# Optimization experiments

Measured on AMD Instinct MI355X. Metric: run time of the kernel, lower is better.

## Reference

```python
import jax, jax.numpy as jnp
import numpy as np

HEADS = 4
HID = 32
IN = 128
OUT = 8
N = 50000
E = 1600000


def setup_inputs() -> dict:
    key = jax.random.key(0)
    ks = jax.random.split(key, 12)
    x = jax.random.normal(ks[0], (N, IN), dtype=jnp.float32)
    edge_index = jax.random.randint(ks[1], (2, E), 0, N, dtype=jnp.int64)
    s = 0.05
    W1 = jax.random.normal(ks[2], (IN, HEADS * HID), dtype=jnp.float32) * s
    att_src1 = jax.random.normal(ks[3], (HEADS, HID), dtype=jnp.float32) * s
    att_dst1 = jax.random.normal(ks[4], (HEADS, HID), dtype=jnp.float32) * s
    b1 = jnp.zeros((HEADS * HID,), dtype=jnp.float32)
    W2 = jax.random.normal(ks[5], (HEADS * HID, HEADS * HID), dtype=jnp.float32) * s
    att_src2 = jax.random.normal(ks[6], (HEADS, HID), dtype=jnp.float32) * s
    att_dst2 = jax.random.normal(ks[7], (HEADS, HID), dtype=jnp.float32) * s
    b2 = jnp.zeros((HEADS * HID,), dtype=jnp.float32)
    Wout = jax.random.normal(ks[8], (HEADS * HID, OUT), dtype=jnp.float32) * s
    bout = jnp.zeros((OUT,), dtype=jnp.float32)
    return {"x": x, "edge_index": edge_index, "W1": W1, "att_src1": att_src1,
            "att_dst1": att_dst1, "b1": b1, "W2": W2, "att_src2": att_src2,
            "att_dst2": att_dst2, "b2": b2, "Wout": Wout, "bout": bout}


def gat_conv(x, src, dst, W, att_src, att_dst, b):
    n = x.shape[0]
    h = (x @ W).reshape(n, HEADS, HID)              # [N,H,C]
    a_s = (h * att_src).sum(-1)                      # [N,H]
    a_d = (h * att_dst).sum(-1)                      # [N,H]
    e = jax.nn.leaky_relu(a_s[src] + a_d[dst], 0.2)  # [E,H]
    # scatter-softmax over incoming edges of each destination node
    m = jax.ops.segment_max(e, dst, num_segments=n)
    e = jnp.exp(e - m[dst])
    denom = jax.ops.segment_sum(e, dst, num_segments=n)
    alpha = e / (denom[dst] + 1e-16)                 # [E,H]
    msg = h[src] * alpha[:, :, None]                 # [E,H,C]
    out = jax.ops.segment_sum(msg, dst, num_segments=n)
    return out.reshape(n, HEADS * HID) + b


def reference(x, edge_index, W1, att_src1, att_dst1, b1, W2, att_src2, att_dst2, b2, Wout, bout):
    n = x.shape[0]
    # GATConv adds self-loops by default
    loops = jnp.arange(n, dtype=edge_index.dtype)
    src = jnp.concatenate([edge_index[0], loops])
    dst = jnp.concatenate([edge_index[1], loops])
    # dropout p=0.6 is identity in eval mode
    h = gat_conv(x, src, dst, W1, att_src1, att_dst1, b1)
    h = jax.nn.elu(h)
    h = gat_conv(h, src, dst, W2, att_src2, att_dst2, b2)
    return h @ Wout + bout
```

## Files before the change

kernel.cpp:

```cpp
#include <hip/hip_runtime.h>
#include <hip/hip_fp16.h>
#include <math.h>

#define N_NODES 50000
#define E_EDGES 1600000
#define NE_TOT  (E_EDGES + N_NODES)

#define BSH 7
#define NBKT ((N_NODES + 127) >> 7)
#define EPW 4096
#define NWA ((NE_TOT + EPW - 1) / EPW)

#define CH 128


__device__ __forceinline__ void gemm_att_body(
    int bid, int t, float* Wl, float* xs,
    const float* __restrict__ X, const float* __restrict__ W,
    const float* __restrict__ attS, const float* __restrict__ attD,
    __half* __restrict__ H16, float* __restrict__ a_s, float* __restrict__ a_d) {
    int g = t >> 5, cl = t & 31, c4 = cl * 4;
    int rowbase = bid * 32;
    float4 acc[4];
    #pragma unroll
    for (int rr = 0; rr < 4; rr++) acc[rr] = make_float4(0.f, 0.f, 0.f, 0.f);

    for (int kp = 0; kp < 2; kp++) {
        __syncthreads();
        #pragma unroll
        for (int j = 0; j < 8; j++) {
            int f4 = t + 256 * j;
            int kk = f4 >> 5, cg = f4 & 31;
            *(float4*)&Wl[kk * 128 + cg * 4] =
                *(const float4*)&W[(kp * 64 + kk) * 128 + cg * 4];
        }
        #pragma unroll
        for (int j = 0; j < 2; j++) {
            int f4 = t + 256 * j;
            int r = f4 >> 4, k4 = f4 & 15;
            int grow = rowbase + r;
            float4 xv = make_float4(0.f, 0.f, 0.f, 0.f);
            if (grow < N_NODES) xv = *(const float4*)&X[grow * 128 + kp * 64 + k4 * 4];
            *(float4*)&xs[r * 64 + k4 * 4] = xv;
        }
        __syncthreads();
        #pragma unroll
        for (int k4 = 0; k4 < 16; k4++) {
            float4 xv[4];
            #pragma unroll
            for (int rr = 0; rr < 4; rr++)
                xv[rr] = *(float4*)&xs[(g * 4 + rr) * 64 + k4 * 4];
            #pragma unroll
            for (int kk = 0; kk < 4; kk++) {
                float4 wv = *(float4*)&Wl[(k4 * 4 + kk) * 128 + c4];
                #pragma unroll
                for (int rr = 0; rr < 4; rr++) {
                    float xc = (kk == 0) ? xv[rr].x : (kk == 1) ? xv[rr].y
                             : (kk == 2) ? xv[rr].z : xv[rr].w;
                    acc[rr].x += xc * wv.x;
                    acc[rr].y += xc * wv.y;
                    acc[rr].z += xc * wv.z;
                    acc[rr].w += xc * wv.w;
                }
            }
        }
    }

    float4 as4 = *(const float4*)&attS[c4];
    float4 ad4 = *(const float4*)&attD[c4];
    int head = cl >> 3;
    #pragma unroll
    for (int rr = 0; rr < 4; rr++) {
        int grow = rowbase + g * 4 + rr;
        float4 a = acc[rr];
        if (grow < N_NODES) {
            __half2 lo = __floats2half2_rn(a.x, a.y);
            __half2 hi = __floats2half2_rn(a.z, a.w);
            uint2 pk;
            pk.x = *(unsigned int*)&lo;
            pk.y = *(unsigned int*)&hi;
            *(uint2*)&H16[(size_t)grow * 128 + c4] = pk;
        }
        float ps = a.x * as4.x + a.y * as4.y + a.z * as4.z + a.w * as4.w;
        float pd = a.x * ad4.x + a.y * ad4.y + a.z * ad4.z + a.w * ad4.w;
        ps += __shfl_xor(ps, 1); ps += __shfl_xor(ps, 2); ps += __shfl_xor(ps, 4);
        pd += __shfl_xor(pd, 1); pd += __shfl_xor(pd, 2); pd += __shfl_xor(pd, 4);
        if ((cl & 7) == 0 && grow < N_NODES) {
            a_s[grow * 4 + head] = ps;
            a_d[grow * 4 + head] = pd;
        }
    }
}

__global__ __launch_bounds__(256) void k_hist_gemm(
    const int* __restrict__ ei, int* __restrict__ histG,
    const float* __restrict__ X, const float* __restrict__ W,
    const float* __restrict__ attS, const float* __restrict__ attD,
    __half* __restrict__ H16, float* __restrict__ a_s, float* __restrict__ a_d) {
    __shared__ __align__(16) char smem[40960];
    int t = threadIdx.x;
    if (blockIdx.x < NWA) {
        int* h = (int*)smem;
        for (int i = t; i < NBKT; i += 256) h[i] = 0;
        __syncthreads();
        int base = blockIdx.x * EPW;
        #pragma unroll 4
        for (int j = 0; j < EPW / 256; j++) {
            int e = base + t + 256 * j;
            if (e < NE_TOT) {
                int d = (e < E_EDGES) ? ei[E_EDGES + e] : (e - E_EDGES);
                atomicAdd(&h[d >> BSH], 1);
            }
        }
        __syncthreads();
        for (int i = t; i < NBKT; i += 256) histG[blockIdx.x * NBKT + i] = h[i];
    } else {
        float* Wl = (float*)smem;
        float* xs = (float*)(smem + 32768);
        gemm_att_body(blockIdx.x - NWA, t, Wl, xs, X, W, attS, attD, H16, a_s, a_d);
    }
}

__global__ __launch_bounds__(256) void k_gemm_att(
    const float* __restrict__ X, const float* __restrict__ W,
    const float* __restrict__ attS, const float* __restrict__ attD,
    __half* __restrict__ H16, float* __restrict__ a_s, float* __restrict__ a_d) {
    __shared__ float Wl[64 * 128];
    __shared__ float xs[32 * 64];
    gemm_att_body(blockIdx.x, threadIdx.x, Wl, xs, X, W, attS, attD, H16, a_s, a_d);
}


__global__ __launch_bounds__(512) void k_bktscan(int* __restrict__ histG,
                                                 int* __restrict__ bktTotal) {
    __shared__ int sh[512];
    int b = blockIdx.x;
    int t = threadIdx.x;
    int v = (t < NWA) ? histG[t * NBKT + b] : 0;
    sh[t] = v;
    __syncthreads();
    for (int d = 1; d < 512; d <<= 1) {
        int x = (t >= d) ? sh[t - d] : 0;
        __syncthreads();
        sh[t] += x;
        __syncthreads();
    }
    if (t < NWA) histG[t * NBKT + b] = sh[t] - v;
    if (t == 511) bktTotal[b] = sh[511];
}

__global__ __launch_bounds__(512) void k_bktbase(const int* __restrict__ bktTotal,
                                                 int* __restrict__ bktBase,
                                                 int* __restrict__ row_start) {
    __shared__ int sc[512];
    int t = threadIdx.x;
    int v = (t < NBKT) ? bktTotal[t] : 0;
    sc[t] = v;
    __syncthreads();
    for (int d = 1; d < 512; d <<= 1) {
        int x = (t >= d) ? sc[t - d] : 0;
        __syncthreads();
        sc[t] += x;
        __syncthreads();
    }
    if (t < NBKT) bktBase[t] = sc[t] - v;
    if (t == NBKT - 1) { bktBase[NBKT] = sc[t]; row_start[N_NODES] = sc[t]; }
}

__global__ __launch_bounds__(256) void k_binscatter(const int* __restrict__ ei,
                                                    const int* __restrict__ histG,
                                                    const int* __restrict__ bktBase,
                                                    unsigned int* __restrict__ pairs) {
    __shared__ int lofs[NBKT];
    int t = threadIdx.x;
    for (int i = t; i < NBKT; i += 256)
        lofs[i] = bktBase[i] + histG[blockIdx.x * NBKT + i];
    __syncthreads();
    int base = blockIdx.x * EPW;
    #pragma unroll 4
    for (int j = 0; j < EPW / 256; j++) {
        int e = base + t + 256 * j;
        if (e < NE_TOT) {
            int s, d;
            if (e < E_EDGES) { s = ei[e]; d = ei[E_EDGES + e]; }
            else             { s = d = e - E_EDGES; }
            int pos = atomicAdd(&lofs[d >> BSH], 1);
            pairs[pos] = ((unsigned int)d << 16) | (unsigned int)s;
        }
    }
}

__global__ __launch_bounds__(256) void k_bucketsort(const unsigned int* __restrict__ pairs,
                                                    const int* __restrict__ bktBase,
                                                    int* __restrict__ row_start,
                                                    unsigned short* __restrict__ col) {
    __shared__ int cnt[1 << BSH];
    __shared__ int sc[1 << BSH];
    __shared__ int cur[1 << BSH];
    int b = blockIdx.x, t = threadIdx.x;
    int nbeg = b << BSH;
    int ebeg = bktBase[b], eend = bktBase[b + 1];
    if (t < (1 << BSH)) cnt[t] = 0;
    __syncthreads();
    for (int j = ebeg + t; j < eend; j += 256)
        atomicAdd(&cnt[(int)(pairs[j] >> 16) - nbeg], 1);
    __syncthreads();
    int v = (t < (1 << BSH)) ? cnt[t] : 0;
    if (t < (1 << BSH)) sc[t] = v;
    __syncthreads();
    for (int d = 1; d < (1 << BSH); d <<= 1) {
        int x = 0;
        if (t < (1 << BSH) && t >= d) x = sc[t - d];
        __syncthreads();
        if (t < (1 << BSH)) sc[t] += x;
        __syncthreads();
    }
    if (t < (1 << BSH)) {
        int pos = ebeg + sc[t] - v;
        cur[t] = pos;
        int node = nbeg + t;
        if (node < N_NODES) row_start[node] = pos;
    }
    __syncthreads();
    for (int j = ebeg + t; j < eend; j += 256) {
        unsigned int p = pairs[j];
        int pos = atomicAdd(&cur[(int)(p >> 16) - nbeg], 1);
        col[pos] = (unsigned short)(p & 0xFFFFu);
    }
}


__device__ inline float sel4(float4 v, int i) {
    float r = v.x;
    if (i == 1) r = v.y;
    if (i == 2) r = v.z;
    if (i == 3) r = v.w;
    return r;
}

__device__ inline float4 expleaky4(float4 a, float4 b) {
    float4 e, p;
    e.x = a.x + b.x; e.x = e.x > 0.f ? e.x : 0.2f * e.x; p.x = __expf(e.x);
    e.y = a.y + b.y; e.y = e.y > 0.f ? e.y : 0.2f * e.y; p.y = __expf(e.y);
    e.z = a.z + b.z; e.z = e.z > 0.f ? e.z : 0.2f * e.z; p.z = __expf(e.z);
    e.w = a.w + b.w; e.w = e.w > 0.f ? e.w : 0.2f * e.w; p.w = __expf(e.w);
    return p;
}

#define ACC8(q, raw)                                              \
    do {                                                          \
        const __half2* hp_ = (const __half2*)&(raw);              \
        float2 f0_ = __half22float2(hp_[0]);                      \
        float2 f1_ = __half22float2(hp_[1]);                      \
        float2 f2_ = __half22float2(hp_[2]);                      \
        float2 f3_ = __half22float2(hp_[3]);                      \
        acc8[0] = fmaf((q), f0_.x, acc8[0]);                      \
        acc8[1] = fmaf((q), f0_.y, acc8[1]);                      \
        acc8[2] = fmaf((q), f1_.x, acc8[2]);                      \
        acc8[3] = fmaf((q), f1_.y, acc8[3]);                      \
        acc8[4] = fmaf((q), f2_.x, acc8[4]);                      \
        acc8[5] = fmaf((q), f2_.y, acc8[5]);                      \
        acc8[6] = fmaf((q), f3_.x, acc8[6]);                      \
        acc8[7] = fmaf((q), f3_.y, acc8[7]);                      \
    } while (0)

template<int MODE>
__global__ __launch_bounds__(128) void k_agg(
    const __half* __restrict__ H16, const float* __restrict__ a_s,
    const float* __restrict__ a_d, const int* __restrict__ row_start,
    const unsigned short* __restrict__ col, const float* __restrict__ bias,
    float* __restrict__ Hout,
    const float* __restrict__ Wout, const float* __restrict__ bout,
    float* __restrict__ out) {
    __shared__ float4 eS[2][CH];
    __shared__ int    sS[2][CH];

    int wid = threadIdx.x >> 6;
    int lane = threadIdx.x & 63;
    int node = blockIdx.x * 2 + wid;
    if (node >= N_NODES) return;

    int eslot = lane >> 4, cl16 = lane & 15, head = cl16 >> 2;

    float wA[8], wB[8], bo0 = 0.f, bo1 = 0.f;
    if (MODE == 0) {
        int o0 = eslot * 2;
        #pragma unroll
        for (int k = 0; k < 8; k++) {
            wA[k] = Wout[(cl16 * 8 + k) * 8 + o0];
            wB[k] = Wout[(cl16 * 8 + k) * 8 + o0 + 1];
        }
        bo0 = bout[o0]; bo1 = bout[o0 + 1];
    }

    int beg = row_start[node], end = row_start[node + 1];
    int deg = end - beg;
    float4 ad4 = *(const float4*)&a_d[node * 4];
    float4* eA = eS[wid];
    int*    srcA = sS[wid];

    float4 s = make_float4(0.f, 0.f, 0.f, 0.f);
    for (int j = beg + lane; j < end; j += 64) {
        int src = (int)col[j];
        float4 av = *(const float4*)&a_s[src * 4];
        float4 p = expleaky4(av, ad4);
        int idx = j - beg;
        if (idx < CH) { srcA[idx] = src; eA[idx] = p; }
        s.x += p.x; s.y += p.y; s.z += p.z; s.w += p.w;
    }
    #pragma unroll
    for (int off = 32; off > 0; off >>= 1) {
        s.x += __shfl_xor(s.x, off);
        s.y += __shfl_xor(s.y, off);
        s.z += __shfl_xor(s.z, off);
        s.w += __shfl_xor(s.w, off);
    }
    float4 inv;
    inv.x = 1.f / (s.x + 1e-16f);
    inv.y = 1.f / (s.y + 1e-16f);
    inv.z = 1.f / (s.z + 1e-16f);
    inv.w = 1.f / (s.w + 1e-16f);

    const __half* hbase = H16 + cl16 * 8;
    const float* pA = (const float*)eA;
    float acc8[8];
    #pragma unroll
    for (int k = 0; k < 8; k++) acc8[k] = 0.f;

    int nst = min(deg, CH);
    int i = eslot;
    for (; i + 28 < nst; i += 32) {
        int sidx[8]; float qv[8]; float4 rv[8];
        #pragma unroll
        for (int k = 0; k < 8; k++) sidx[k] = srcA[i + 4 * k];
        #pragma unroll
        for (int k = 0; k < 8; k++) qv[k] = pA[(i + 4 * k) * 4 + head];
        #pragma unroll
        for (int k = 0; k < 8; k++)
            rv[k] = *(const float4*)(hbase + (size_t)sidx[k] * 128);
        #pragma unroll
        for (int k = 0; k < 8; k++) ACC8(qv[k], rv[k]);
    }
    for (; i + 12 < nst; i += 16) {
        int s0 = srcA[i];
        int s1 = srcA[i + 4];
        int s2 = srcA[i + 8];
        int s3 = srcA[i + 12];
        float q0 = pA[i * 4 + head];
        float q1 = pA[(i + 4) * 4 + head];
        float q2 = pA[(i + 8) * 4 + head];
        float q3 = pA[(i + 12) * 4 + head];
        float4 r0 = *(const float4*)(hbase + (size_t)s0 * 128);
        float4 r1 = *(const float4*)(hbase + (size_t)s1 * 128);
        float4 r2 = *(const float4*)(hbase + (size_t)s2 * 128);
        float4 r3 = *(const float4*)(hbase + (size_t)s3 * 128);
        ACC8(q0, r0);
        ACC8(q1, r1);
        ACC8(q2, r2);
        ACC8(q3, r3);
    }
    for (; i < nst; i += 4) {
        int src = srcA[i];
        float p = pA[i * 4 + head];
        float4 raw = *(const float4*)(hbase + (size_t)src * 128);
        ACC8(p, raw);
    }
    for (int cb = beg + CH; cb < end; cb += CH) {
        int cnt = min(end - cb, CH);
        for (int idx = lane; idx < cnt; idx += 64) {
            int src = (int)col[cb + idx];
            float4 av = *(const float4*)&a_s[src * 4];
            float4 p = expleaky4(av, ad4);
            srcA[idx] = src; eA[idx] = p;
        }
        for (int ii = eslot; ii < cnt; ii += 4) {
            int src = srcA[ii];
            float p = pA[ii * 4 + head];
            float4 raw = *(const float4*)(hbase + (size_t)src * 128);
            ACC8(p, raw);
        }
    }

    #pragma unroll
    for (int k = 0; k < 8; k++) {
        acc8[k] += __shfl_xor(acc8[k], 16);
        acc8[k] += __shfl_xor(acc8[k], 32);
    }

    float ih = sel4(inv, head);
    if (MODE == 1) {
        if (eslot == 0) {
            const float* bp = &bias[cl16 * 8];
            float o[8];
            #pragma unroll
            for (int k = 0; k < 8; k++) {
                o[k] = acc8[k] * ih + bp[k];
                o[k] = o[k] > 0.f ? o[k] : expm1f(o[k]);
            }
            float* op = &Hout[(size_t)node * 128 + cl16 * 8];
            *(float4*)&op[0] = make_float4(o[0], o[1], o[2], o[3]);
            *(float4*)&op[4] = make_float4(o[4], o[5], o[6], o[7]);
        }
    } else {
        const float* bp = &bias[cl16 * 8];
        float h2[8];
        #pragma unroll
        for (int k = 0; k < 8; k++) h2[k] = acc8[k] * ih + bp[k];
        float p0 = 0.f, p1 = 0.f;
        #pragma unroll
        for (int k = 0; k < 8; k++) {
            p0 = fmaf(h2[k], wA[k], p0);
            p1 = fmaf(h2[k], wB[k], p1);
        }
        #pragma unroll
        for (int d = 1; d <= 8; d <<= 1) {
            p0 += __shfl_xor(p0, d);
            p1 += __shfl_xor(p1, d);
        }
        if (cl16 == 0) {
            int o0 = eslot * 2;
            float2 ov = make_float2(p0 + bo0, p1 + bo1);
            *(float2*)&out[(size_t)node * 8 + o0] = ov;
        }
    }
}


extern "C" void kernel_launch(void* const* d_in, const int* in_sizes, int n_in,
                              void* d_out, int out_size, void* d_ws, size_t ws_size,
                              hipStream_t stream) {
    const float* x     = (const float*)d_in[0];
    const int*   ei    = (const int*)d_in[1];
    const float* W1    = (const float*)d_in[2];
    const float* attS1 = (const float*)d_in[3];
    const float* attD1 = (const float*)d_in[4];
    const float* b1    = (const float*)d_in[5];
    const float* W2    = (const float*)d_in[6];
    const float* attS2 = (const float*)d_in[7];
    const float* attD2 = (const float*)d_in[8];
    const float* b2    = (const float*)d_in[9];
    const float* Wout  = (const float*)d_in[10];
    const float* bout  = (const float*)d_in[11];
    float* out = (float*)d_out;

    char* ws = (char*)d_ws;
    size_t off = 0;
    auto alloc = [&](size_t bytes) -> void* {
        void* p = ws + off;
        off += (bytes + 255) & ~(size_t)255;
        return p;
    };
    float*          hB        = (float*)alloc((size_t)N_NODES * 128 * 4);
    __half*         h16       = (__half*)alloc((size_t)N_NODES * 128 * 2);
    float*          a_s       = (float*)alloc((size_t)N_NODES * 4 * 4);
    float*          a_d       = (float*)alloc((size_t)N_NODES * 4 * 4);
    int*            row_start = (int*)alloc((size_t)(N_NODES + 1) * 4);
    unsigned short* col       = (unsigned short*)alloc((size_t)NE_TOT * 2);
    int*            histG     = (int*)alloc((size_t)NWA * NBKT * 4);
    int*            bktTotal  = (int*)alloc((size_t)NBKT * 4);
    int*            bktBase   = (int*)alloc((size_t)(NBKT + 1) * 4);
    unsigned int*   pairs     = (unsigned int*)hB;

    int nbG = (N_NODES + 31) / 32;
    int nbA = (N_NODES + 1) / 2;

    k_hist_gemm<<<NWA + nbG, 256, 0, stream>>>(ei, histG, x, W1, attS1, attD1,
                                               h16, a_s, a_d);
    k_bktscan<<<NBKT, 512, 0, stream>>>(histG, bktTotal);
    k_bktbase<<<1, 512, 0, stream>>>(bktTotal, bktBase, row_start);
    k_binscatter<<<NWA, 256, 0, stream>>>(ei, histG, bktBase, pairs);
    k_bucketsort<<<NBKT, 256, 0, stream>>>(pairs, bktBase, row_start, col);

    k_agg<1><<<nbA, 128, 0, stream>>>(h16, a_s, a_d, row_start, col, b1, hB,
                                      Wout, bout, out);
    k_gemm_att<<<nbG, 256, 0, stream>>>(hB, W2, attS2, attD2, h16, a_s, a_d);
    k_agg<0><<<nbA, 128, 0, stream>>>(h16, a_s, a_d, row_start, col, b2, hB,
                                      Wout, bout, out);
}
```

Measured before the change: 286.9 us.

## Split each node's aggregation across two wavefronts with shared-memory reduction

The aggregation kernel now assigns two 64-lane wavefronts per destination node, in 256-thread blocks holding two nodes. The softmax denominator and feature accumulators are combined through shared memory. Overflow chunks for high-degree nodes are processed in lockstep with block-wide barriers. The output projection is computed only by the first wavefront's 16 lanes, reading Wout directly. This roughly doubles memory-level parallelism per node for the gather-bound loop, at the cost of added __syncthreads, a smaller unroll (4 loads per lane instead of 8), and idle lanes during the final projection.

```diff
diff --git a/kernel.cpp b/kernel.cpp
--- a/kernel.cpp
+++ b/kernel.cpp
@@ -265,7 +265,7 @@
     } while (0)
 
 template<int MODE>
-__global__ __launch_bounds__(128) void k_agg(
+__global__ __launch_bounds__(256) void k_agg(
     const __half* __restrict__ H16, const float* __restrict__ a_s,
     const float* __restrict__ a_d, const int* __restrict__ row_start,
     const unsigned short* __restrict__ col, const float* __restrict__ bias,
@@ -274,33 +274,24 @@
     float* __restrict__ out) {
     __shared__ float4 eS[2][CH];
     __shared__ int    sS[2][CH];
-
-    int wid = threadIdx.x >> 6;
+    __shared__ float  red[2][16][8];
+    __shared__ float4 sRed[2][2];
+    __shared__ int    chk[2];
+
+    int wv = threadIdx.x >> 6;
+    int nodeSlot = wv >> 1;
+    int wpair = wv & 1;
     int lane = threadIdx.x & 63;
-    int node = blockIdx.x * 2 + wid;
-    if (node >= N_NODES) return;
-
-    int eslot = lane >> 4, cl16 = lane & 15, head = cl16 >> 2;
-
-    float wA[8], wB[8], bo0 = 0.f, bo1 = 0.f;
-    if (MODE == 0) {
-        int o0 = eslot * 2;
-        #pragma unroll
-        for (int k = 0; k < 8; k++) {
-            wA[k] = Wout[(cl16 * 8 + k) * 8 + o0];
-            wB[k] = Wout[(cl16 * 8 + k) * 8 + o0 + 1];
-        }
-        bo0 = bout[o0]; bo1 = bout[o0 + 1];
-    }
+    int node = blockIdx.x * 2 + nodeSlot;
 
     int beg = row_start[node], end = row_start[node + 1];
     int deg = end - beg;
     float4 ad4 = *(const float4*)&a_d[node * 4];
-    float4* eA = eS[wid];
-    int*    srcA = sS[wid];
+    float4* eA = eS[nodeSlot];
+    int*    srcA = sS[nodeSlot];
 
     float4 s = make_float4(0.f, 0.f, 0.f, 0.f);
-    for (int j = beg + lane; j < end; j += 64) {
+    for (int j = beg + wpair * 64 + lane; j < end; j += 128) {
         int src = (int)col[j];
         float4 av = *(const float4*)&a_s[src * 4];
         float4 p = expleaky4(av, ad4);
@@ -315,12 +306,21 @@
         s.z += __shfl_xor(s.z, off);
         s.w += __shfl_xor(s.w, off);
     }
+    int myc = (deg > CH) ? (deg - CH + CH - 1) / CH : 0;
+    if (lane == 0) {
+        sRed[nodeSlot][wpair] = s;
+        if (wpair == 0) chk[nodeSlot] = myc;
+    }
+    __syncthreads();
+    float4 s0 = sRed[nodeSlot][0], s1 = sRed[nodeSlot][1];
     float4 inv;
-    inv.x = 1.f / (s.x + 1e-16f);
-    inv.y = 1.f / (s.y + 1e-16f);
-    inv.z = 1.f / (s.z + 1e-16f);
-    inv.w = 1.f / (s.w + 1e-16f);
-
+    inv.x = 1.f / (s0.x + s1.x + 1e-16f);
+    inv.y = 1.f / (s0.y + s1.y + 1e-16f);
+    inv.z = 1.f / (s0.z + s1.z + 1e-16f);
+    inv.w = 1.f / (s0.w + s1.w + 1e-16f);
+    int maxc = max(chk[0], chk[1]);
+
+    int slot8 = wpair * 4 + (lane >> 4), cl16 = lane & 15, head = cl16 >> 2;
     const __half* hbase = H16 + cl16 * 8;
     const float* pA = (const float*)eA;
     float acc8[8];
@@ -328,56 +328,52 @@
     for (int k = 0; k < 8; k++) acc8[k] = 0.f;
 
     int nst = min(deg, CH);
-    int i = eslot;
-    for (; i + 28 < nst; i += 32) {
-        int sidx[8]; float qv[8]; float4 rv[8];
-        #pragma unroll
-        for (int k = 0; k < 8; k++) sidx[k] = srcA[i + 4 * k];
-        #pragma unroll
-        for (int k = 0; k < 8; k++) qv[k] = pA[(i + 4 * k) * 4 + head];
-        #pragma unroll
-        for (int k = 0; k < 8; k++)
-            rv[k] = *(const float4*)(hbase + (size_t)sidx[k] * 128);
-        #pragma unroll
-        for (int k = 0; k < 8; k++) ACC8(qv[k], rv[k]);
-    }
-    for (; i + 12 < nst; i += 16) {
-        int s0 = srcA[i];
-        int s1 = srcA[i + 4];
-        int s2 = srcA[i + 8];
-        int s3 = srcA[i + 12];
+    int i = slot8;
+    for (; i + 24 < nst; i += 32) {
+        int t0 = srcA[i];
+        int t1 = srcA[i + 8];
+        int t2 = srcA[i + 16];
+        int t3 = srcA[i + 24];
         float q0 = pA[i * 4 + head];
-        float q1 = pA[(i + 4) * 4 + head];
-        float q2 = pA[(i + 8) * 4 + head];
-        float q3 = pA[(i + 12) * 4 + head];
-        float4 r0 = *(const float4*)(hbase + (size_t)s0 * 128);
-        float4 r1 = *(const float4*)(hbase + (size_t)s1 * 128);
-        float4 r2 = *(const float4*)(hbase + (size_t)s2 * 128);
-        float4 r3 = *(const float4*)(hbase + (size_t)s3 * 128);
+        float q1 = pA[(i + 8) * 4 + head];
+        float q2 = pA[(i + 16) * 4 + head];
+        float q3 = pA[(i + 24) * 4 + head];
+        float4 r0 = *(const float4*)(hbase + (size_t)t0 * 128);
+        float4 r1 = *(const float4*)(hbase + (size_t)t1 * 128);
+        float4 r2 = *(const float4*)(hbase + (size_t)t2 * 128);
+        float4 r3 = *(const float4*)(hbase + (size_t)t3 * 128);
         ACC8(q0, r0);
         ACC8(q1, r1);
         ACC8(q2, r2);
         ACC8(q3, r3);
     }
-    for (; i < nst; i += 4) {
+    for (; i < nst; i += 8) {
         int src = srcA[i];
         float p = pA[i * 4 + head];
         float4 raw = *(const float4*)(hbase + (size_t)src * 128);
         ACC8(p, raw);
     }
-    for (int cb = beg + CH; cb < end; cb += CH) {
-        int cnt = min(end - cb, CH);
-        for (int idx = lane; idx < cnt; idx += 64) {
-            int src = (int)col[cb + idx];
-            float4 av = *(const float4*)&a_s[src * 4];
-            float4 p = expleaky4(av, ad4);
-            srcA[idx] = src; eA[idx] = p;
-        }
-        for (int ii = eslot; ii < cnt; ii += 4) {
-            int src = srcA[ii];
-            float p = pA[ii * 4 + head];
-            float4 raw = *(const float4*)(hbase + (size_t)src * 128);
-            ACC8(p, raw);
+    for (int c = 0; c < maxc; c++) {
+        __syncthreads();
+        int cb = beg + CH + c * CH;
+        if (c < myc) {
+            int cnt = min(end - cb, CH);
+            for (int idx = wpair * 64 + lane; idx < cnt; idx += 128) {
+                int src = (int)col[cb + idx];
+                float4 av = *(const float4*)&a_s[src * 4];
+                float4 p = expleaky4(av, ad4);
+                srcA[idx] = src; eA[idx] = p;
+            }
+        }
+        __syncthreads();
+        if (c < myc) {
+            int cnt = min(end - cb, CH);
+            for (int ii = slot8; ii < cnt; ii += 8) {
+                int src = srcA[ii];
+                float p = pA[ii * 4 + head];
+                float4 raw = *(const float4*)(hbase + (size_t)src * 128);
+                ACC8(p, raw);
+            }
         }
     }
 
@@ -386,10 +382,16 @@
         acc8[k] += __shfl_xor(acc8[k], 16);
         acc8[k] += __shfl_xor(acc8[k], 32);
     }
-
-    float ih = sel4(inv, head);
-    if (MODE == 1) {
-        if (eslot == 0) {
+    if (wpair == 1 && lane < 16) {
+        #pragma unroll
+        for (int k = 0; k < 8; k++) red[nodeSlot][lane][k] = acc8[k];
+    }
+    __syncthreads();
+    if (wpair == 0 && lane < 16) {
+        #pragma unroll
+        for (int k = 0; k < 8; k++) acc8[k] += red[nodeSlot][lane][k];
+        float ih = sel4(inv, head);
+        if (MODE == 1) {
             const float* bp = &bias[cl16 * 8];
             float o[8];
             #pragma unroll
@@ -400,27 +402,30 @@
             float* op = &Hout[(size_t)node * 128 + cl16 * 8];
             *(float4*)&op[0] = make_float4(o[0], o[1], o[2], o[3]);
             *(float4*)&op[4] = make_float4(o[4], o[5], o[6], o[7]);
-        }
-    } else {
-        const float* bp = &bias[cl16 * 8];
-        float h2[8];
-        #pragma unroll
-        for (int k = 0; k < 8; k++) h2[k] = acc8[k] * ih + bp[k];
-        float p0 = 0.f, p1 = 0.f;
-        #pragma unroll
-        for (int k = 0; k < 8; k++) {
-            p0 = fmaf(h2[k], wA[k], p0);
-            p1 = fmaf(h2[k], wB[k], p1);
-        }
-        #pragma unroll
-        for (int d = 1; d <= 8; d <<= 1) {
-            p0 += __shfl_xor(p0, d);
-            p1 += __shfl_xor(p1, d);
-        }
-        if (cl16 == 0) {
-            int o0 = eslot * 2;
-            float2 ov = make_float2(p0 + bo0, p1 + bo1);
-            *(float2*)&out[(size_t)node * 8 + o0] = ov;
+        } else {
+            const float* bp = &bias[cl16 * 8];
+            float h2[8];
+            #pragma unroll
+            for (int k = 0; k < 8; k++) h2[k] = acc8[k] * ih + bp[k];
+            float po[8];
+            #pragma unroll
+            for (int o = 0; o < 8; o++) {
+                float t = 0.f;
+                #pragma unroll
+                for (int k = 0; k < 8; k++)
+                    t = fmaf(h2[k], Wout[(cl16 * 8 + k) * 8 + o], t);
+                po[o] = t;
+            }
+            #pragma unroll
+            for (int d = 1; d <= 8; d <<= 1) {
+                #pragma unroll
+                for (int o = 0; o < 8; o++) po[o] += __shfl_xor(po[o], d);
+            }
+            if (lane == 0) {
+                #pragma unroll
+                for (int o = 0; o < 8; o++)
+                    out[(size_t)node * 8 + o] = po[o] + bout[o];
+            }
         }
     }
 }
@@ -462,7 +467,7 @@
     unsigned int*   pairs     = (unsigned int*)hB;
 
     int nbG = (N_NODES + 31) / 32;
-    int nbA = (N_NODES + 1) / 2;
+    int nbA = N_NODES / 2;
 
     k_hist_gemm<<<NWA + nbG, 256, 0, stream>>>(ei, histG, x, W1, attS1, attD1,
                                                h16, a_s, a_d);
@@ -471,9 +476,9 @@
     k_binscatter<<<NWA, 256, 0, stream>>>(ei, histG, bktBase, pairs);
     k_bucketsort<<<NBKT, 256, 0, stream>>>(pairs, bktBase, row_start, col);
 
-    k_agg<1><<<nbA, 128, 0, stream>>>(h16, a_s, a_d, row_start, col, b1, hB,
+    k_agg<1><<<nbA, 256, 0, stream>>>(h16, a_s, a_d, row_start, col, b1, hB,
                                       Wout, bout, out);
     k_gemm_att<<<nbG, 256, 0, stream>>>(hB, W2, attS2, attD2, h16, a_s, a_d);
-    k_agg<0><<<nbA, 128, 0, stream>>>(h16, a_s, a_d, row_start, col, b2, hB,
+    k_agg<0><<<nbA, 256, 0, stream>>>(h16, a_s, a_d, row_start, col, b2, hB,
                                       Wout, bout, out);
 }
```

Result: slower. 316.2 us (+10.2%).
